# Optimization experiments

Measured on AMD Instinct MI355X. Metric: run time of the kernel, lower is better.

## Reference

```python
import jax, jax.numpy as jnp
import numpy as np

N_NODES = 100000
N_EDGES = 1_600_000
F_IN, HID, N_CLS = 128, 64, 32
NEG_SLOPE = 0.2  # PyG GATv2Conv default


def _segment_softmax(scores, seg, num_segments):
    # numerically stable softmax over edges grouped by destination node
    m = jax.ops.segment_max(scores, seg, num_segments=num_segments)
    ex = jnp.exp(scores - m[seg])
    s = jax.ops.segment_sum(ex, seg, num_segments=num_segments)
    return ex / (s[seg] + 1e-16)


def _gatv2_layer(x, src, dst, Wl, bl, Wr, br, att, bias, num_nodes):
    xl = x @ Wl + bl              # source transform  [N, C]
    xr = x @ Wr + br              # target transform  [N, C]
    # per-edge GATv2 attention logit: a . leaky_relu(xl_j + xr_i)
    e = jax.nn.leaky_relu(xl[src] + xr[dst], NEG_SLOPE) @ att  # [E]
    alpha = _segment_softmax(e, dst, num_nodes)                 # [E]
    out = jax.ops.segment_sum(alpha[:, None] * xl[src], dst, num_segments=num_nodes)
    return out + bias


def _add_self_loops(edge_index, n):
    loops = jnp.arange(n, dtype=edge_index.dtype)
    return jnp.concatenate([edge_index, jnp.stack([loops, loops])], axis=1)


def setup_inputs() -> dict:
    key = jax.random.key(0)
    ks = jax.random.split(key, 8)
    s1 = 1.0 / np.sqrt(F_IN)
    s2 = 1.0 / np.sqrt(HID)
    return {
        "x": jax.random.normal(ks[0], (N_NODES, F_IN), jnp.float32),
        "edge_index": jax.random.randint(ks[1], (2, N_EDGES), 0, N_NODES, jnp.int64),
        "W1l": jax.random.normal(ks[2], (F_IN, HID), jnp.float32) * s1,
        "b1l": jnp.zeros((HID,), jnp.float32),
        "W1r": jax.random.normal(ks[3], (F_IN, HID), jnp.float32) * s1,
        "b1r": jnp.zeros((HID,), jnp.float32),
        "att1": jax.random.normal(ks[4], (HID,), jnp.float32) * s2,
        "bias1": jnp.zeros((HID,), jnp.float32),
        "W2l": jax.random.normal(ks[5], (HID, N_CLS), jnp.float32) * s2,
        "b2l": jnp.zeros((N_CLS,), jnp.float32),
        "W2r": jax.random.normal(ks[6], (HID, N_CLS), jnp.float32) * s2,
        "b2r": jnp.zeros((N_CLS,), jnp.float32),
        "att2": jax.random.normal(ks[7], (N_CLS,), jnp.float32) / np.sqrt(N_CLS),
        "bias2": jnp.zeros((N_CLS,), jnp.float32),
    }


def reference(x, edge_index, W1l, b1l, W1r, b1r, att1, bias1,
              W2l, b2l, W2r, b2r, att2, bias2):
    n = x.shape[0]
    ei = _add_self_loops(edge_index, n)
    src, dst = ei[0], ei[1]
    h = jax.nn.relu(_gatv2_layer(x, src, dst, W1l, b1l, W1r, b1r, att1, bias1, n))
    # F.dropout(training=False) is identity in eval mode
    out = _gatv2_layer(h, src, dst, W2l, b2l, W2r, b2r, att2, bias2, n)
    return out
```

## Files before the change

### kernel.cpp

```cpp
#include <hip/hip_runtime.h>
#include <hip/hip_fp16.h>
#include <math.h>

#define F_IN 128
#define HID 64
#define NCLS 32
#define NEG 0.2f
#define NBKT 256
#define CHUNK 8192

using bf8 = __attribute__((ext_vector_type(8))) short;
using f4v = __attribute__((ext_vector_type(4))) float;
typedef _Float16 hv2 __attribute__((ext_vector_type(2)));

__device__ __forceinline__ void f4fma(float4& a, float s, const float4& w) {
    a.x = fmaf(s, w.x, a.x);
    a.y = fmaf(s, w.y, a.y);
    a.z = fmaf(s, w.z, a.z);
    a.w = fmaf(s, w.w, a.w);
}
__device__ __forceinline__ unsigned short f2bf(float f) {
    unsigned u = __float_as_uint(f);
    return (unsigned short)((u + 0x7FFFu + ((u >> 16) & 1u)) >> 16);
}
__device__ __forceinline__ unsigned short f2h(float f) {
    return __half_as_ushort(__float2half(f));
}
__device__ __forceinline__ float h2f(unsigned short u) {
    return __half2float(__ushort_as_half(u));
}
__device__ __forceinline__ unsigned pkaddabs(unsigned a, unsigned b) {
    hv2 r = __builtin_bit_cast(hv2, a) + __builtin_bit_cast(hv2, b);
    return __builtin_bit_cast(unsigned, r) & 0x7FFF7FFFu;
}
__device__ __forceinline__ float fdot2(unsigned a, unsigned b, float c) {
    return __builtin_amdgcn_fdot2(__builtin_bit_cast(hv2, a),
                                  __builtin_bit_cast(hv2, b), c, false);
}
__device__ __forceinline__ float h2lo(unsigned a) {
    return (float)__builtin_bit_cast(hv2, a).x;
}
__device__ __forceinline__ float h2hi(unsigned a) {
    return (float)__builtin_bit_cast(hv2, a).y;
}
template <int CTRL>
__device__ __forceinline__ float dpp_add(float v) {
    int t = __builtin_amdgcn_update_dpp(0, __float_as_int(v), CTRL, 0xf, 0xf, true);
    return v + __int_as_float(t);
}


__global__ __launch_bounds__(256) void bucketHist(const int* __restrict__ ei,
                                                  int Eorig, int Etot,
                                                  int* __restrict__ bucketSize, int BK) {
    __shared__ int h[512];
    int t = threadIdx.x;
    for (int j = t; j < BK; j += 256) h[j] = 0;
    __syncthreads();
    int base = blockIdx.x * CHUNK;
    int end = base + CHUNK < Etot ? base + CHUNK : Etot;
    for (int i = base + t; i < end; i += 256) {
        int dst = i < Eorig ? ei[Eorig + i] : i - Eorig;
        atomicAdd(&h[dst >> 8], 1);
    }
    __syncthreads();
    for (int j = t; j < BK; j += 256)
        if (h[j]) atomicAdd(&bucketSize[j], h[j]);
}

__global__ __launch_bounds__(256) void bucketScan(const int* __restrict__ bucketSize,
                                                  int* __restrict__ bucketStart,
                                                  int* __restrict__ bucketCursor,
                                                  int BK, int Etot) {
    __shared__ int sd[256];
    int t = threadIdx.x;
    int v0 = (2 * t     < BK) ? bucketSize[2 * t]     : 0;
    int v1 = (2 * t + 1 < BK) ? bucketSize[2 * t + 1] : 0;
    int ts = v0 + v1;
    sd[t] = ts;
    __syncthreads();
    for (int off = 1; off < 256; off <<= 1) {
        int x = (t >= off) ? sd[t - off] : 0;
        __syncthreads();
        sd[t] += x;
        __syncthreads();
    }
    int excl = sd[t] - ts;
    if (2 * t < BK)     { bucketStart[2 * t] = excl;          bucketCursor[2 * t] = excl; }
    if (2 * t + 1 < BK) { bucketStart[2 * t + 1] = excl + v0; bucketCursor[2 * t + 1] = excl + v0; }
    if (t == 255) bucketStart[BK] = Etot;
}

__global__ __launch_bounds__(256) void bucketScatter(const int* __restrict__ ei,
                                                     int Eorig, int Etot,
                                                     int* __restrict__ bucketCursor,
                                                     int* __restrict__ pairs, int BK) {
    __shared__ int h[512], lbase[512], hcur[512];
    int t = threadIdx.x;
    for (int j = t; j < BK; j += 256) { h[j] = 0; hcur[j] = 0; }
    __syncthreads();
    int base = blockIdx.x * CHUNK;
    int end = base + CHUNK < Etot ? base + CHUNK : Etot;
    for (int i = base + t; i < end; i += 256) {
        int dst = i < Eorig ? ei[Eorig + i] : i - Eorig;
        atomicAdd(&h[dst >> 8], 1);
    }
    __syncthreads();
    for (int j = t; j < BK; j += 256)
        lbase[j] = h[j] ? atomicAdd(&bucketCursor[j], h[j]) : 0;
    __syncthreads();
    for (int i = base + t; i < end; i += 256) {
        int src, dst;
        if (i < Eorig) { src = ei[i]; dst = ei[Eorig + i]; }
        else           { src = dst = i - Eorig; }
        int b = dst >> 8;
        int off = atomicAdd(&hcur[b], 1);
        pairs[lbase[b] + off] = (src << 8) | (dst & 255);
    }
}

__global__ __launch_bounds__(256) void bucketCSR(const int* __restrict__ pairs,
                                                 const int* __restrict__ bucketStart,
                                                 int* __restrict__ rowstart,
                                                 int* __restrict__ cnt,
                                                 int* __restrict__ srclist, int N) {
    __shared__ int c[256], cur[256];
    int t = threadIdx.x;
    int b = blockIdx.x;
    int lo = b * NBKT;
    int eb = bucketStart[b], ee = bucketStart[b + 1];
    c[t] = 0;
    __syncthreads();
    for (int i = eb + t; i < ee; i += 256)
        atomicAdd(&c[pairs[i] & 255], 1);
    __syncthreads();
    cur[t] = c[t];
    __syncthreads();
    for (int off = 1; off < 256; off <<= 1) {
        int x = (t >= off) ? cur[t - off] : 0;
        __syncthreads();
        cur[t] += x;
        __syncthreads();
    }
    int excl = cur[t] - c[t];
    int node = lo + t;
    if (node < N) { rowstart[node] = eb + excl; cnt[node] = c[t]; }
    __syncthreads();
    cur[t] = excl;
    __syncthreads();
    for (int i = eb + t; i < ee; i += 256) {
        int v = pairs[i];
        int pos = atomicAdd(&cur[v & 255], 1);
        srclist[eb + pos] = v >> 8;
    }
}

__global__ __launch_bounds__(256) void prepW(const float* __restrict__ Wl,
                                             const float* __restrict__ Wr,
                                             const float* __restrict__ att1,
                                             const float* __restrict__ att2,
                                             uint4* __restrict__ wfrag,
                                             unsigned short* __restrict__ att1h,
                                             unsigned short* __restrict__ att2h) {
    int e = blockIdx.x * 256 + threadIdx.x;
    if (e >= 2048) {
        int i = e - 2048;
        if (i < HID) att1h[i] = f2h(att1[i]);
        else if (i < HID + NCLS) att2h[i - HID] = f2h(att2[i - HID]);
        return;
    }
    int lane = e & 63;
    int kt = (e >> 6) & 3;
    int ct = (e >> 8) & 3;
    int mat = e >> 10;
    const float* W = mat ? Wr : Wl;
    int k0 = kt * 32 + (lane >> 4) * 8;
    int c = ct * 16 + (lane & 15);
    unsigned short h[8];
#pragma unroll
    for (int j = 0; j < 8; j++) h[j] = f2bf(W[(k0 + j) * HID + c]);
    wfrag[e] = *(uint4*)h;
}

__global__ __launch_bounds__(256) void transform1(const float* __restrict__ x,
                                                  const uint4* __restrict__ wfrag,
                                                  const float* __restrict__ bl,
                                                  const float* __restrict__ br,
                                                  const float* __restrict__ att,
                                                  unsigned short* __restrict__ xlh,
                                                  unsigned short* __restrict__ xrh,
                                                  float* __restrict__ sl, int N) {
    __shared__ uint4 sw[2048];
    int t = threadIdx.x;
#pragma unroll
    for (int j = 0; j < 8; j++) sw[t + j * 256] = wfrag[t + j * 256];
    __syncthreads();

    int w = t >> 6, lane = t & 63;
    int nb = blockIdx.x * 64 + w * 16;
    int m = lane & 15, quad = lane >> 4;

    int arow = nb + m; if (arow >= N) arow = N - 1;
    const float* xrow = x + (size_t)arow * F_IN + quad * 8;
    bf8 afr[4];
#pragma unroll
    for (int kt = 0; kt < 4; kt++) {
        float4 lo = *(const float4*)(xrow + kt * 32);
        float4 hi = *(const float4*)(xrow + kt * 32 + 4);
        unsigned short hh[8];
        hh[0] = f2bf(lo.x); hh[1] = f2bf(lo.y); hh[2] = f2bf(lo.z); hh[3] = f2bf(lo.w);
        hh[4] = f2bf(hi.x); hh[5] = f2bf(hi.y); hh[6] = f2bf(hi.z); hh[7] = f2bf(hi.w);
        afr[kt] = *(bf8*)hh;
    }

    float am[4];
#pragma unroll
    for (int ct = 0; ct < 4; ct++) am[ct] = att[ct * 16 + m];
    float slp[4] = {0.f, 0.f, 0.f, 0.f};

#pragma unroll
    for (int mat = 0; mat < 2; mat++) {
        const float* bias = mat ? br : bl;
#pragma unroll
        for (int ct = 0; ct < 4; ct++) {
            f4v acc = {0.f, 0.f, 0.f, 0.f};
#pragma unroll
            for (int kt = 0; kt < 4; kt++) {
                bf8 bfr = *(bf8*)&sw[((mat * 4 + ct) * 4 + kt) * 64 + lane];
                acc = __builtin_amdgcn_mfma_f32_16x16x32_bf16(afr[kt], bfr, acc, 0, 0, 0);
            }
            int ch = ct * 16 + m;
            float bv = bias[ch];
#pragma unroll
            for (int reg = 0; reg < 4; reg++) {
                int node = nb + quad * 4 + reg;
                float o = acc[reg] + bv;
                if (mat) {
                    if (node < N) xrh[(size_t)node * HID + ch] = f2h(o);
                } else {
                    unsigned short hb = f2h(o);
                    slp[reg] = fmaf(am[ct], h2f(hb), slp[reg]);
                    if (node < N) xlh[(size_t)node * HID + ch] = hb;
                }
            }
        }
    }
#pragma unroll
    for (int o2 = 1; o2 < 16; o2 <<= 1) {
#pragma unroll
        for (int reg = 0; reg < 4; reg++) slp[reg] += __shfl_xor(slp[reg], o2, 64);
    }
    if (m == 0) {
#pragma unroll
        for (int reg = 0; reg < 4; reg++) {
            int node = nb + quad * 4 + reg;
            if (node < N) sl[node] = 0.6f * slp[reg];
        }
    }
}

__global__ __launch_bounds__(256) void transform2(const float* __restrict__ h,
                                                  const float* __restrict__ Wl,
                                                  const float* __restrict__ bl,
                                                  const float* __restrict__ Wr,
                                                  const float* __restrict__ br,
                                                  const float* __restrict__ att,
                                                  unsigned short* __restrict__ xlh,
                                                  unsigned short* __restrict__ xrh,
                                                  float* __restrict__ sl, int N) {
    __shared__ float sWl[HID * NCLS];
    __shared__ float sWr[HID * NCLS];
    __shared__ float sx[128][68];
    int t = threadIdx.x;
    int nb = blockIdx.x * 128;

#pragma unroll
    for (int j = 0; j < 2; j++) {
        int f = t + j * 256;
        ((float4*)sWl)[f] = ((const float4*)Wl)[f];
        ((float4*)sWr)[f] = ((const float4*)Wr)[f];
    }
    int maxf = (N - nb) * 16;
#pragma unroll
    for (int j = 0; j < 8; j++) {
        int f = t + j * 256;
        int node = f >> 4, kc = f & 15;
        float4 v = {0.f, 0.f, 0.f, 0.f};
        if (f < maxf) v = ((const float4*)(h + (size_t)nb * HID))[f];
        v.x = fmaxf(v.x, 0.f);
        v.y = fmaxf(v.y, 0.f);
        v.z = fmaxf(v.z, 0.f);
        v.w = fmaxf(v.w, 0.f);
        *(float4*)&sx[node][kc * 4] = v;
    }
    __syncthreads();

    int c4 = (t & 7) * 4;
    int slot = t >> 3;
    float4 bl4 = *(const float4*)(bl + c4);
    float4 br4 = *(const float4*)(br + c4);
    float4 at4 = *(const float4*)(att + c4);
    float4 accl[4] = {bl4, bl4, bl4, bl4};
    float4 accr[4] = {br4, br4, br4, br4};

#pragma unroll 4
    for (int k4 = 0; k4 < HID / 4; k4++) {
        int k = k4 * 4;
        float4 wl0 = *(const float4*)&sWl[(k + 0) * NCLS + c4];
        float4 wl1 = *(const float4*)&sWl[(k + 1) * NCLS + c4];
        float4 wl2 = *(const float4*)&sWl[(k + 2) * NCLS + c4];
        float4 wl3 = *(const float4*)&sWl[(k + 3) * NCLS + c4];
        float4 wr0 = *(const float4*)&sWr[(k + 0) * NCLS + c4];
        float4 wr1 = *(const float4*)&sWr[(k + 1) * NCLS + c4];
        float4 wr2 = *(const float4*)&sWr[(k + 2) * NCLS + c4];
        float4 wr3 = *(const float4*)&sWr[(k + 3) * NCLS + c4];
#pragma unroll
        for (int j = 0; j < 4; j++) {
            float4 xv = *(const float4*)&sx[slot + j * 32][k];
            f4fma(accl[j], xv.x, wl0); f4fma(accr[j], xv.x, wr0);
            f4fma(accl[j], xv.y, wl1); f4fma(accr[j], xv.y, wr1);
            f4fma(accl[j], xv.z, wl2); f4fma(accr[j], xv.z, wr2);
            f4fma(accl[j], xv.w, wl3); f4fma(accr[j], xv.w, wr3);
        }
    }
#pragma unroll
    for (int j = 0; j < 4; j++) {
        ushort4 o;
        o.x = f2h(accl[j].x); o.y = f2h(accl[j].y);
        o.z = f2h(accl[j].z); o.w = f2h(accl[j].w);
        ushort4 orr;
        orr.x = f2h(accr[j].x); orr.y = f2h(accr[j].y);
        orr.z = f2h(accr[j].z); orr.w = f2h(accr[j].w);
        float slpj = fmaf(at4.x, h2f(o.x),
                     fmaf(at4.y, h2f(o.y),
                     fmaf(at4.z, h2f(o.z), at4.w * h2f(o.w))));
        slpj += __shfl_xor(slpj, 1, 64);
        slpj += __shfl_xor(slpj, 2, 64);
        slpj += __shfl_xor(slpj, 4, 64);
        int g = nb + slot + j * 32;
        if (g < N) {
            *(ushort4*)(xlh + (size_t)g * NCLS + c4) = o;
            *(ushort4*)(xrh + (size_t)g * NCLS + c4) = orr;
            if ((t & 7) == 0) sl[g] = 0.6f * slpj;
        }
    }
}

#define LOADROW(VP, SRC)                                                  \
    {                                                                     \
        const unsigned short* rp = xlh + (unsigned)(SRC) * C + cb0;       \
        if (NH == 4) *(uint4*)(VP) = *(const uint4*)rp;                   \
        else         *(uint2*)(VP) = *(const uint2*)rp;                   \
    }

template <int C>
__global__ __launch_bounds__(256) void fusedAggF(const unsigned short* __restrict__ xlh,
                                                 const unsigned short* __restrict__ xrh,
                                                 const unsigned short* __restrict__ atth,
                                                 const float* __restrict__ sl,
                                                 const int* __restrict__ rowstart,
                                                 const int* __restrict__ cnt,
                                                 const int* __restrict__ srclist,
                                                 const float* __restrict__ bias,
                                                 float* __restrict__ out, int N) {
    constexpr int CH = C / 8;
    constexpr int NH = CH / 2;
    int wid = threadIdx.x >> 6;
    int lane = threadIdx.x & 63;
    int n = blockIdx.x * 4 + wid;
    if (n >= N) return;

    int slot = lane & 7;
    int pos  = lane >> 3;
    int cb0  = pos * CH;

    unsigned xrp[NH], atp[NH];
    if (NH == 4) {
        *(uint4*)xrp = *(const uint4*)(xrh + (size_t)n * C + cb0);
        *(uint4*)atp = *(const uint4*)(atth + cb0);
    } else {
        *(uint2*)xrp = *(const uint2*)(xrh + (size_t)n * C + cb0);
        *(uint2*)atp = *(const uint2*)(atth + cb0);
    }

    int row = rowstart[n];
    int deg = cnt[n];

    float s = 0.f;
    float acc[CH];
#pragma unroll
    for (int c = 0; c < CH; c++) acc[c] = 0.f;

    for (int cb = 0; cb < deg; cb += 64) {
        int len = deg - cb; if (len > 64) len = 64;
        int len1 = len - 1;
        int li = lane < len ? lane : len1;
        int srcv = srclist[row + cb + li];
        float slv = sl[srcv];
        int nbatch = (len + 7) >> 3;

        int e0 = min(slot, len1);
        float tA = __shfl(slv, e0, 64);
        int srcA = __shfl(srcv, e0, 64);
        unsigned vpA[NH];
        LOADROW(vpA, srcA)

        for (int b = 0; b < nbatch; b++) {
            unsigned vpN[NH];
            float tN = 0.f;
            bool more = (b + 1 < nbatch);
            if (more) {
                int eN = min((b + 1) * 8 + slot, len1);
                tN = __shfl(slv, eN, 64);
                int srcN = __shfl(srcv, eN, 64);
                LOADROW(vpN, srcN)
            }
            float pa = 0.f;
#pragma unroll
            for (int j = 0; j < NH; j++)
                pa = fdot2(pkaddabs(vpA[j], xrp[j]), atp[j], pa);
            pa = dpp_add<0x128>(pa);
            pa += __shfl_xor(pa, 16, 64);
            pa += __shfl_xor(pa, 32, 64);
            float wgt = (b * 8 + slot < len) ? __expf(fmaf(0.4f, pa, tA)) : 0.f;
            s += wgt;
#pragma unroll
            for (int j = 0; j < NH; j++) {
                acc[2 * j]     = fmaf(wgt, h2lo(vpA[j]), acc[2 * j]);
                acc[2 * j + 1] = fmaf(wgt, h2hi(vpA[j]), acc[2 * j + 1]);
            }
            if (more) {
#pragma unroll
                for (int j = 0; j < NH; j++) vpA[j] = vpN[j];
                tA = tN;
            }
        }
    }
#pragma unroll
    for (int c = 0; c < CH; c++) {
        acc[c] = dpp_add<0xB1>(acc[c]);
        acc[c] = dpp_add<0x4E>(acc[c]);
        acc[c] = dpp_add<0x141>(acc[c]);
    }
    s = dpp_add<0xB1>(s);
    s = dpp_add<0x4E>(s);
    s = dpp_add<0x141>(s);

    if (slot == 0) {
        float inv = 1.f / (s + 1e-16f);
        float o8[CH];
        float bi[CH];
        if (NH == 4) {
            *(float4*)&bi[0] = *(const float4*)(bias + cb0);
            *(float4*)&bi[4] = *(const float4*)(bias + cb0 + 4);
        } else {
            *(float4*)&bi[0] = *(const float4*)(bias + cb0);
        }
#pragma unroll
        for (int c = 0; c < CH; c++) o8[c] = fmaf(acc[c], inv, bi[c]);
        if (NH == 4) {
            *(float4*)(out + (size_t)n * C + cb0)     = *(float4*)&o8[0];
            *(float4*)(out + (size_t)n * C + cb0 + 4) = *(float4*)&o8[4];
        } else {
            *(float4*)(out + (size_t)n * C + cb0) = *(float4*)&o8[0];
        }
    }
}

extern "C" void kernel_launch(void* const* d_in, const int* in_sizes, int n_in,
                              void* d_out, int out_size, void* d_ws, size_t ws_size,
                              hipStream_t stream) {
    const float* x     = (const float*)d_in[0];
    const int*   ei    = (const int*)d_in[1];
    const float* W1l   = (const float*)d_in[2];
    const float* b1l   = (const float*)d_in[3];
    const float* W1r   = (const float*)d_in[4];
    const float* b1r   = (const float*)d_in[5];
    const float* att1  = (const float*)d_in[6];
    const float* bias1 = (const float*)d_in[7];
    const float* W2l   = (const float*)d_in[8];
    const float* b2l   = (const float*)d_in[9];
    const float* W2r   = (const float*)d_in[10];
    const float* b2r   = (const float*)d_in[11];
    const float* att2  = (const float*)d_in[12];
    const float* bias2 = (const float*)d_in[13];
    float* out = (float*)d_out;

    int N     = in_sizes[0] / F_IN;
    int Eorig = in_sizes[1] / 2;
    int Etot  = Eorig + N;
    int BK    = (N + NBKT - 1) / NBKT;

    char* p = (char*)d_ws;
    auto alloc = [&](size_t bytes) { void* r = (void*)p; p += (bytes + 255) & ~(size_t)255; return r; };
    unsigned short* xl1h = (unsigned short*)alloc((size_t)N * HID * 2);
    unsigned short* xr1h = (unsigned short*)alloc((size_t)N * HID * 2);
    float* h       = (float*)alloc((size_t)N * HID * 4);
    unsigned short* xl2h = (unsigned short*)alloc((size_t)N * NCLS * 2);
    unsigned short* xr2h = (unsigned short*)alloc((size_t)N * NCLS * 2);
    int*   cnt     = (int*)alloc((size_t)N * 4);
    int*   rowstart= (int*)alloc((size_t)N * 4);
    int*   srclist = (int*)alloc((size_t)Etot * 4);
    uint4* wfrag   = (uint4*)alloc(2048 * 16);
    float* sl1     = (float*)alloc((size_t)N * 4);
    float* sl2     = (float*)alloc((size_t)N * 4);
    unsigned short* att1h = (unsigned short*)alloc(HID * 2);
    unsigned short* att2h = (unsigned short*)alloc(NCLS * 2);
    int*   bucketSize   = (int*)alloc(520 * 4);
    int*   bucketStart  = (int*)alloc(520 * 4);
    int*   bucketCursor = (int*)alloc(520 * 4);
    int*   pairs   = (int*)h;

    int nChunks = (Etot + CHUNK - 1) / CHUNK;

    hipMemsetAsync(bucketSize, 0, 520 * 4, stream);
    bucketHist<<<nChunks, 256, 0, stream>>>(ei, Eorig, Etot, bucketSize, BK);
    bucketScan<<<1, 256, 0, stream>>>(bucketSize, bucketStart, bucketCursor, BK, Etot);
    bucketScatter<<<nChunks, 256, 0, stream>>>(ei, Eorig, Etot, bucketCursor, pairs, BK);
    bucketCSR<<<BK, 256, 0, stream>>>(pairs, bucketStart, rowstart, cnt, srclist, N);

    prepW<<<9, 256, 0, stream>>>(W1l, W1r, att1, att2, wfrag, att1h, att2h);
    transform1<<<(N + 63) / 64, 256, 0, stream>>>(x, wfrag, b1l, b1r, att1, xl1h, xr1h, sl1, N);
    fusedAggF<HID><<<(N + 3) / 4, 256, 0, stream>>>(xl1h, xr1h, att1h, sl1, rowstart, cnt,
                                                    srclist, bias1, h, N);

    transform2<<<(N + 127) / 128, 256, 0, stream>>>(h, W2l, b2l, W2r, b2r, att2, xl2h, xr2h, sl2, N);
    fusedAggF<NCLS><<<(N + 3) / 4, 256, 0, stream>>>(xl2h, xr2h, att2h, sl2, rowstart, cnt,
                                                     srclist, bias2, out, N);
}
```

Baseline: 302.7 us.

## Ping-pong edge row buffers, shrink CSR buckets, and use DPP reductions

The aggregation loop now alternates between two register buffers for prefetched source rows. This removes the per-iteration copy of the next row into the current one and drops the clamp on the prefetch lane index. The CSR build uses 128-node buckets with half-size edge chunks, which gives more blocks and smaller shared-memory counting, and the single-block scan now handles four buckets per thread. Shuffle-based reductions in both transform kernels are replaced with DPP adds. Without the clamp, the prefetch can read rows for lanes past the segment length; this relies on masked weights and on those lanes holding valid indices.

```diff
diff --git a/kernel.cpp b/kernel.cpp
--- a/kernel.cpp
+++ b/kernel.cpp
@@ -6,8 +6,10 @@
 #define HID 64
 #define NCLS 32
 #define NEG 0.2f
-#define NBKT 256
-#define CHUNK 8192
+#define NBKT 128
+#define BSH 7
+#define BMSK 127
+#define CHUNK 4096
 
 using bf8 = __attribute__((ext_vector_type(8))) short;
 using f4v = __attribute__((ext_vector_type(4))) float;
@@ -53,7 +55,7 @@
 __global__ __launch_bounds__(256) void bucketHist(const int* __restrict__ ei,
                                                   int Eorig, int Etot,
                                                   int* __restrict__ bucketSize, int BK) {
-    __shared__ int h[512];
+    __shared__ int h[1024];
     int t = threadIdx.x;
     for (int j = t; j < BK; j += 256) h[j] = 0;
     __syncthreads();
@@ -61,7 +63,7 @@
     int end = base + CHUNK < Etot ? base + CHUNK : Etot;
     for (int i = base + t; i < end; i += 256) {
         int dst = i < Eorig ? ei[Eorig + i] : i - Eorig;
-        atomicAdd(&h[dst >> 8], 1);
+        atomicAdd(&h[dst >> BSH], 1);
     }
     __syncthreads();
     for (int j = t; j < BK; j += 256)
@@ -74,9 +76,12 @@
                                                   int BK, int Etot) {
     __shared__ int sd[256];
     int t = threadIdx.x;
-    int v0 = (2 * t     < BK) ? bucketSize[2 * t]     : 0;
-    int v1 = (2 * t + 1 < BK) ? bucketSize[2 * t + 1] : 0;
-    int ts = v0 + v1;
+    int v[4]; int ts = 0;
+#pragma unroll
+    for (int k = 0; k < 4; k++) {
+        v[k] = (4 * t + k < BK) ? bucketSize[4 * t + k] : 0;
+        ts += v[k];
+    }
     sd[t] = ts;
     __syncthreads();
     for (int off = 1; off < 256; off <<= 1) {
@@ -86,8 +91,11 @@
         __syncthreads();
     }
     int excl = sd[t] - ts;
-    if (2 * t < BK)     { bucketStart[2 * t] = excl;          bucketCursor[2 * t] = excl; }
-    if (2 * t + 1 < BK) { bucketStart[2 * t + 1] = excl + v0; bucketCursor[2 * t + 1] = excl + v0; }
+#pragma unroll
+    for (int k = 0; k < 4; k++) {
+        if (4 * t + k < BK) { bucketStart[4 * t + k] = excl; bucketCursor[4 * t + k] = excl; }
+        excl += v[k];
+    }
     if (t == 255) bucketStart[BK] = Etot;
 }
 
@@ -95,7 +103,7 @@
                                                      int Eorig, int Etot,
                                                      int* __restrict__ bucketCursor,
                                                      int* __restrict__ pairs, int BK) {
-    __shared__ int h[512], lbase[512], hcur[512];
+    __shared__ int h[1024], lbase[1024], hcur[1024];
     int t = threadIdx.x;
     for (int j = t; j < BK; j += 256) { h[j] = 0; hcur[j] = 0; }
     __syncthreads();
@@ -103,7 +111,7 @@
     int end = base + CHUNK < Etot ? base + CHUNK : Etot;
     for (int i = base + t; i < end; i += 256) {
         int dst = i < Eorig ? ei[Eorig + i] : i - Eorig;
-        atomicAdd(&h[dst >> 8], 1);
+        atomicAdd(&h[dst >> BSH], 1);
     }
     __syncthreads();
     for (int j = t; j < BK; j += 256)
@@ -113,9 +121,9 @@
         int src, dst;
         if (i < Eorig) { src = ei[i]; dst = ei[Eorig + i]; }
         else           { src = dst = i - Eorig; }
-        int b = dst >> 8;
+        int b = dst >> BSH;
         int off = atomicAdd(&hcur[b], 1);
-        pairs[lbase[b] + off] = (src << 8) | (dst & 255);
+        pairs[lbase[b] + off] = (src << BSH) | (dst & BMSK);
     }
 }
 
@@ -132,7 +140,7 @@
     c[t] = 0;
     __syncthreads();
     for (int i = eb + t; i < ee; i += 256)
-        atomicAdd(&c[pairs[i] & 255], 1);
+        atomicAdd(&c[pairs[i] & BMSK], 1);
     __syncthreads();
     cur[t] = c[t];
     __syncthreads();
@@ -144,14 +152,14 @@
     }
     int excl = cur[t] - c[t];
     int node = lo + t;
-    if (node < N) { rowstart[node] = eb + excl; cnt[node] = c[t]; }
+    if (t < NBKT && node < N) { rowstart[node] = eb + excl; cnt[node] = c[t]; }
     __syncthreads();
     cur[t] = excl;
     __syncthreads();
     for (int i = eb + t; i < ee; i += 256) {
         int v = pairs[i];
-        int pos = atomicAdd(&cur[v & 255], 1);
-        srclist[eb + pos] = v >> 8;
+        int pos = atomicAdd(&cur[v & BMSK], 1);
+        srclist[eb + pos] = v >> BSH;
     }
 }
 
@@ -246,9 +254,11 @@
         }
     }
 #pragma unroll
-    for (int o2 = 1; o2 < 16; o2 <<= 1) {
-#pragma unroll
-        for (int reg = 0; reg < 4; reg++) slp[reg] += __shfl_xor(slp[reg], o2, 64);
+    for (int reg = 0; reg < 4; reg++) {
+        slp[reg] = dpp_add<0xB1>(slp[reg]);
+        slp[reg] = dpp_add<0x4E>(slp[reg]);
+        slp[reg] = dpp_add<0x141>(slp[reg]);
+        slp[reg] = dpp_add<0x140>(slp[reg]);
     }
     if (m == 0) {
 #pragma unroll
@@ -334,9 +344,9 @@
         float slpj = fmaf(at4.x, h2f(o.x),
                      fmaf(at4.y, h2f(o.y),
                      fmaf(at4.z, h2f(o.z), at4.w * h2f(o.w))));
-        slpj += __shfl_xor(slpj, 1, 64);
-        slpj += __shfl_xor(slpj, 2, 64);
-        slpj += __shfl_xor(slpj, 4, 64);
+        slpj = dpp_add<0xB1>(slpj);
+        slpj = dpp_add<0x4E>(slpj);
+        slpj = dpp_add<0x141>(slpj);
         int g = nb + slot + j * 32;
         if (g < N) {
             *(ushort4*)(xlh + (size_t)g * NCLS + c4) = o;
@@ -353,8 +363,27 @@
         else         *(uint2*)(VP) = *(const uint2*)rp;                   \
     }
 
+#define COMPUTE(VP, T, B)                                                 \
+    {                                                                     \
+        float pa = 0.f;                                                   \
+        _Pragma("unroll")                                                 \
+        for (int j = 0; j < NH; j++)                                      \
+            pa = fdot2(pkaddabs((VP)[j], xrp[j]), atp[j], pa);            \
+        pa = dpp_add<0x128>(pa);                                          \
+        pa += __shfl_xor(pa, 16, 64);                                     \
+        pa += __shfl_xor(pa, 32, 64);                                     \
+        float wgt = ((B) * 8 + slot < len) ? __expf(fmaf(0.4f, pa, (T)))  \
+                                           : 0.f;                         \
+        s += wgt;                                                         \
+        _Pragma("unroll")                                                 \
+        for (int j = 0; j < NH; j++) {                                    \
+            acc[2 * j]     = fmaf(wgt, h2lo((VP)[j]), acc[2 * j]);        \
+            acc[2 * j + 1] = fmaf(wgt, h2hi((VP)[j]), acc[2 * j + 1]);    \
+        }                                                                 \
+    }
+
 template <int C>
-__global__ __launch_bounds__(256) void fusedAggF(const unsigned short* __restrict__ xlh,
+__global__ __launch_bounds__(256) void fusedAggG(const unsigned short* __restrict__ xlh,
                                                  const unsigned short* __restrict__ xrh,
                                                  const unsigned short* __restrict__ atth,
                                                  const float* __restrict__ sl,
@@ -399,41 +428,33 @@
         float slv = sl[srcv];
         int nbatch = (len + 7) >> 3;
 
-        int e0 = min(slot, len1);
-        float tA = __shfl(slv, e0, 64);
-        int srcA = __shfl(srcv, e0, 64);
-        unsigned vpA[NH];
+        float tA = __shfl(slv, slot, 64);
+        int srcA = __shfl(srcv, slot, 64);
+        unsigned vpA[NH], vpB[NH];
+        float tB;
         LOADROW(vpA, srcA)
 
-        for (int b = 0; b < nbatch; b++) {
-            unsigned vpN[NH];
-            float tN = 0.f;
-            bool more = (b + 1 < nbatch);
-            if (more) {
-                int eN = min((b + 1) * 8 + slot, len1);
-                tN = __shfl(slv, eN, 64);
-                int srcN = __shfl(srcv, eN, 64);
-                LOADROW(vpN, srcN)
+        int b = 0;
+        while (true) {
+            bool moreB = (b + 1 < nbatch);
+            if (moreB) {
+                int e = (b + 1) * 8 + slot;
+                tB = __shfl(slv, e, 64);
+                int srcB = __shfl(srcv, e, 64);
+                LOADROW(vpB, srcB)
             }
-            float pa = 0.f;
-#pragma unroll
-            for (int j = 0; j < NH; j++)
-                pa = fdot2(pkaddabs(vpA[j], xrp[j]), atp[j], pa);
-            pa = dpp_add<0x128>(pa);
-            pa += __shfl_xor(pa, 16, 64);
-            pa += __shfl_xor(pa, 32, 64);
-            float wgt = (b * 8 + slot < len) ? __expf(fmaf(0.4f, pa, tA)) : 0.f;
-            s += wgt;
-#pragma unroll
-            for (int j = 0; j < NH; j++) {
-                acc[2 * j]     = fmaf(wgt, h2lo(vpA[j]), acc[2 * j]);
-                acc[2 * j + 1] = fmaf(wgt, h2hi(vpA[j]), acc[2 * j + 1]);
+            COMPUTE(vpA, tA, b)
+            if (!moreB) break;
+            bool moreA = (b + 2 < nbatch);
+            if (moreA) {
+                int e = (b + 2) * 8 + slot;
+                tA = __shfl(slv, e, 64);
+                int srcA2 = __shfl(srcv, e, 64);
+                LOADROW(vpA, srcA2)
             }
-            if (more) {
-#pragma unroll
-                for (int j = 0; j < NH; j++) vpA[j] = vpN[j];
-                tA = tN;
-            }
+            COMPUTE(vpB, tB, b + 1)
+            if (!moreA) break;
+            b += 2;
         }
     }
 #pragma unroll
@@ -506,14 +527,14 @@
     float* sl2     = (float*)alloc((size_t)N * 4);
     unsigned short* att1h = (unsigned short*)alloc(HID * 2);
     unsigned short* att2h = (unsigned short*)alloc(NCLS * 2);
-    int*   bucketSize   = (int*)alloc(520 * 4);
-    int*   bucketStart  = (int*)alloc(520 * 4);
-    int*   bucketCursor = (int*)alloc(520 * 4);
+    int*   bucketSize   = (int*)alloc(1040 * 4);
+    int*   bucketStart  = (int*)alloc(1040 * 4);
+    int*   bucketCursor = (int*)alloc(1040 * 4);
     int*   pairs   = (int*)h;
 
     int nChunks = (Etot + CHUNK - 1) / CHUNK;
 
-    hipMemsetAsync(bucketSize, 0, 520 * 4, stream);
+    hipMemsetAsync(bucketSize, 0, 1040 * 4, stream);
     bucketHist<<<nChunks, 256, 0, stream>>>(ei, Eorig, Etot, bucketSize, BK);
     bucketScan<<<1, 256, 0, stream>>>(bucketSize, bucketStart, bucketCursor, BK, Etot);
     bucketScatter<<<nChunks, 256, 0, stream>>>(ei, Eorig, Etot, bucketCursor, pairs, BK);
@@ -521,10 +542,10 @@
 
     prepW<<<9, 256, 0, stream>>>(W1l, W1r, att1, att2, wfrag, att1h, att2h);
     transform1<<<(N + 63) / 64, 256, 0, stream>>>(x, wfrag, b1l, b1r, att1, xl1h, xr1h, sl1, N);
-    fusedAggF<HID><<<(N + 3) / 4, 256, 0, stream>>>(xl1h, xr1h, att1h, sl1, rowstart, cnt,
+    fusedAggG<HID><<<(N + 3) / 4, 256, 0, stream>>>(xl1h, xr1h, att1h, sl1, rowstart, cnt,
                                                     srclist, bias1, h, N);
 
     transform2<<<(N + 127) / 128, 256, 0, stream>>>(h, W2l, b2l, W2r, b2r, att2, xl2h, xr2h, sl2, N);
-    fusedAggF<NCLS><<<(N + 3) / 4, 256, 0, stream>>>(xl2h, xr2h, att2h, sl2, rowstart, cnt,
+    fusedAggG<NCLS><<<(N + 3) / 4, 256, 0, stream>>>(xl2h, xr2h, att2h, sl2, rowstart, cnt,
                                                      srclist, bias2, out, N);
 }
```

After: 298.9 us. No clear change (-1.3%).
